# Performance work log

Measured on AMD Instinct MI355X. Metric: run time of the kernel, lower is better.

Reference implementation:

```python
import jax, jax.numpy as jnp
import numpy as np

B, S, V, M = 8, 512, 32000, 32
PAD_ID = 1


def setup_inputs() -> dict:
    key = jax.random.key(0)
    k1, k2, k3 = jax.random.split(key, 3)
    logits = jax.random.normal(k1, (B, S, V), dtype=jnp.float32)
    a = jax.random.randint(k2, (B, S), 0, V, dtype=jnp.int64)
    mask = jax.random.randint(k3, (B, S, M), 0, V, dtype=jnp.int64)
    return {"logits": logits, "a": a, "mask": mask}


def reference(logits, a, mask):
    # softmax over vocab: prob[b,s,v]
    prob = jax.nn.softmax(logits, axis=-1)
    # _base: masked gather + segment-sum over candidate ids (>0 are valid)
    gathered = jnp.take_along_axis(prob, mask, axis=-1)      # [B,S,M]
    valid = (mask > 0).astype(prob.dtype)
    base = (gathered * valid).sum(-1)                         # [B,S]
    # prob of the taken action token (equiv. to one_hot * prob sum)
    p_a = jnp.take_along_axis(prob, a[..., None], axis=-1)[..., 0]  # [B,S]
    logp = jnp.log(p_a / base)
    pad_mask = (a != PAD_ID).astype(prob.dtype)
    return (logp * pad_mask).sum(-1)                          # [B]
```

## Files before the change

kernel.cpp:

```cpp
#include <hip/hip_runtime.h>
#include <hip/hip_bf16.h>
#include <math.h>


#define BB 8
#define SS 512
#define VV 32000
#define MM 32

__global__ void init_out_kernel(float* out) {
    if (threadIdx.x < BB) out[threadIdx.x] = 0.0f;
}

__global__ __launch_bounds__(256) void logp_kernel(
    const float* __restrict__ logits,
    const int*   __restrict__ a,
    const int*   __restrict__ mask,
    float*       __restrict__ out)
{
    const int wave = threadIdx.x >> 6;
    const int lane = threadIdx.x & 63;
    const int pos  = (blockIdx.x << 2) + wave;
    const int b    = pos >> 9;

    const float* __restrict__ row = logits + (size_t)pos * VV;

    const int aid = a[pos];
    const float logit_a = row[aid];

    float x = -INFINITY;
    if (lane < MM) {
        const int m = mask[pos * MM + lane];
        if (m > 0) x = row[m];
    }

    float mx = x;
    #pragma unroll
    for (int off = 32; off; off >>= 1)
        mx = fmaxf(mx, __shfl_xor(mx, off, 64));

    float e = (x == -INFINITY) ? 0.0f : expf(x - mx);
    #pragma unroll
    for (int off = 32; off; off >>= 1)
        e += __shfl_xor(e, off, 64);

    const float lse  = mx + logf(e);
    const float logp = (aid != 1) ? (logit_a - lse) : 0.0f;

    __shared__ float ws[4];
    if (lane == 0) ws[wave] = logp;
    __syncthreads();
    if (threadIdx.x == 0) {
        const float s = ws[0] + ws[1] + ws[2] + ws[3];
        atomicAdd(&out[b], s);
    }
}

extern "C" void kernel_launch(void* const* d_in, const int* in_sizes, int n_in,
                              void* d_out, int out_size, void* d_ws, size_t ws_size,
                              hipStream_t stream) {
    const float* logits = (const float*)d_in[0];
    const int*   a      = (const int*)d_in[1];
    const int*   mask   = (const int*)d_in[2];
    float*       out    = (float*)d_out;

    init_out_kernel<<<1, 64, 0, stream>>>(out);

    const int n_pos  = BB * SS;
    const int blocks = n_pos / 4;
    logp_kernel<<<blocks, 256, 0, stream>>>(logits, a, mask, out);
}
```

Before: 564.5 us.

## Fuse output init into one block-per-batch kernel with per-position loop

```diff
diff --git a/kernel.cpp b/kernel.cpp
--- a/kernel.cpp
+++ b/kernel.cpp
@@ -8,51 +8,63 @@
 #define VV 32000
 #define MM 32
 
-__global__ void init_out_kernel(float* out) {
-    if (threadIdx.x < BB) out[threadIdx.x] = 0.0f;
-}
-
-__global__ __launch_bounds__(256) void logp_kernel(
+__global__ __launch_bounds__(1024) void logp_fused_kernel(
     const float* __restrict__ logits,
     const int*   __restrict__ a,
     const int*   __restrict__ mask,
     float*       __restrict__ out)
 {
+    const int b    = blockIdx.x;
     const int wave = threadIdx.x >> 6;
     const int lane = threadIdx.x & 63;
-    const int pos  = (blockIdx.x << 2) + wave;
-    const int b    = pos >> 9;
+    const int hl   = lane & 31;
+    const int half = lane >> 5;
 
-    const float* __restrict__ row = logits + (size_t)pos * VV;
+    const int pos_base = b * SS + wave * 32 + half;
 
-    const int aid = a[pos];
-    const float logit_a = row[aid];
+    float acc = 0.0f;
 
-    float x = -INFINITY;
-    if (lane < MM) {
-        const int m = mask[pos * MM + lane];
-        if (m > 0) x = row[m];
+    int m_cur = mask[pos_base * MM + hl];
+    int a_cur = a[pos_base];
+
+    #pragma unroll
+    for (int i = 0; i < 16; ++i) {
+        const int pos = pos_base + 2 * i;
+        const float* __restrict__ row = logits + (size_t)pos * VV;
+
+        float x  = (m_cur > 0) ? row[m_cur] : -INFINITY;
+        float la = row[a_cur];
+        const int a_hold = a_cur;
+
+        if (i < 15) {
+            m_cur = mask[(pos + 2) * MM + hl];
+            a_cur = a[pos + 2];
+        }
+
+        float mx = x;
+        #pragma unroll
+        for (int off = 16; off; off >>= 1)
+            mx = fmaxf(mx, __shfl_xor(mx, off, 64));
+
+        float e = (x == -INFINITY) ? 0.0f : expf(x - mx);
+        #pragma unroll
+        for (int off = 16; off; off >>= 1)
+            e += __shfl_xor(e, off, 64);
+
+        const float lse = mx + logf(e);
+        if (hl == 0 && a_hold != 1) acc += la - lse;
     }
 
-    float mx = x;
-    #pragma unroll
-    for (int off = 32; off; off >>= 1)
-        mx = fmaxf(mx, __shfl_xor(mx, off, 64));
+    acc += __shfl_xor(acc, 32, 64);
 
-    float e = (x == -INFINITY) ? 0.0f : expf(x - mx);
-    #pragma unroll
-    for (int off = 32; off; off >>= 1)
-        e += __shfl_xor(e, off, 64);
-
-    const float lse  = mx + logf(e);
-    const float logp = (aid != 1) ? (logit_a - lse) : 0.0f;
-
-    __shared__ float ws[4];
-    if (lane == 0) ws[wave] = logp;
+    __shared__ float wsum[16];
+    if (lane == 0) wsum[wave] = acc;
     __syncthreads();
     if (threadIdx.x == 0) {
-        const float s = ws[0] + ws[1] + ws[2] + ws[3];
-        atomicAdd(&out[b], s);
+        float s = 0.0f;
+        #pragma unroll
+        for (int w = 0; w < 16; ++w) s += wsum[w];
+        out[b] = s;
     }
 }
 
@@ -64,9 +76,5 @@
     const int*   mask   = (const int*)d_in[2];
     float*       out    = (float*)d_out;
 
-    init_out_kernel<<<1, 64, 0, stream>>>(out);
-
-    const int n_pos  = BB * SS;
-    const int blocks = n_pos / 4;
-    logp_kernel<<<blocks, 256, 0, stream>>>(logits, a, mask, out);
+    logp_fused_kernel<<<BB, 1024, 0, stream>>>(logits, a, mask, out);
 }
```

After: 594.3 us. 1.05x slower.

## Assign one block per batch row and one thread per position, dropping atomics

Applied to the files above, without the earlier changes.

```diff
diff --git a/kernel.cpp b/kernel.cpp
--- a/kernel.cpp
+++ b/kernel.cpp
@@ -8,51 +8,62 @@
 #define VV 32000
 #define MM 32
 
-__global__ void init_out_kernel(float* out) {
-    if (threadIdx.x < BB) out[threadIdx.x] = 0.0f;
-}
-
-__global__ __launch_bounds__(256) void logp_kernel(
+__global__ __launch_bounds__(512) void logp_kernel(
     const float* __restrict__ logits,
     const int*   __restrict__ a,
     const int*   __restrict__ mask,
     float*       __restrict__ out)
 {
-    const int wave = threadIdx.x >> 6;
-    const int lane = threadIdx.x & 63;
-    const int pos  = (blockIdx.x << 2) + wave;
-    const int b    = pos >> 9;
+    const int b   = blockIdx.x;
+    const int t   = threadIdx.x;
+    const int pos = b * SS + t;
 
     const float* __restrict__ row = logits + (size_t)pos * VV;
 
-    const int aid = a[pos];
-    const float logit_a = row[aid];
-
-    float x = -INFINITY;
-    if (lane < MM) {
-        const int m = mask[pos * MM + lane];
-        if (m > 0) x = row[m];
+    const int a_id = a[pos];
+    int m[MM];
+    const int4* __restrict__ mrow = reinterpret_cast<const int4*>(mask + (size_t)pos * MM);
+    #pragma unroll
+    for (int q = 0; q < MM / 4; ++q) {
+        const int4 v = mrow[q];
+        m[4 * q + 0] = v.x; m[4 * q + 1] = v.y;
+        m[4 * q + 2] = v.z; m[4 * q + 3] = v.w;
     }
 
-    float mx = x;
+    float x[MM];
+    #pragma unroll
+    for (int j = 0; j < MM; ++j) {
+        const int idx = (m[j] > 0) ? m[j] : 0;
+        x[j] = row[idx];
+    }
+    const float logit_a = row[a_id];
+
+    float mx = -INFINITY;
+    #pragma unroll
+    for (int j = 0; j < MM; ++j)
+        mx = fmaxf(mx, (m[j] > 0) ? x[j] : -INFINITY);
+
+    float e = 0.0f;
+    #pragma unroll
+    for (int j = 0; j < MM; ++j)
+        e += (m[j] > 0) ? expf(x[j] - mx) : 0.0f;
+
+    const float lse  = mx + logf(e);
+    float logp = (a_id != 1) ? (logit_a - lse) : 0.0f;
+
     #pragma unroll
     for (int off = 32; off; off >>= 1)
-        mx = fmaxf(mx, __shfl_xor(mx, off, 64));
+        logp += __shfl_xor(logp, off, 64);
 
-    float e = (x == -INFINITY) ? 0.0f : expf(x - mx);
-    #pragma unroll
-    for (int off = 32; off; off >>= 1)
-        e += __shfl_xor(e, off, 64);
-
-    const float lse  = mx + logf(e);
-    const float logp = (aid != 1) ? (logit_a - lse) : 0.0f;
-
-    __shared__ float ws[4];
-    if (lane == 0) ws[wave] = logp;
+    __shared__ float wsum[8];
+    const int wave = t >> 6;
+    if ((t & 63) == 0) wsum[wave] = logp;
     __syncthreads();
-    if (threadIdx.x == 0) {
-        const float s = ws[0] + ws[1] + ws[2] + ws[3];
-        atomicAdd(&out[b], s);
+    if (t == 0) {
+        float s = 0.0f;
+        #pragma unroll
+        for (int w = 0; w < 8; ++w) s += wsum[w];
+        out[b] = s;
     }
 }
 
@@ -64,9 +75,5 @@
     const int*   mask   = (const int*)d_in[2];
     float*       out    = (float*)d_out;
 
-    init_out_kernel<<<1, 64, 0, stream>>>(out);
-
-    const int n_pos  = BB * SS;
-    const int blocks = n_pos / 4;
-    logp_kernel<<<blocks, 256, 0, stream>>>(logits, a, mask, out);
+    logp_kernel<<<BB, SS, 0, stream>>>(logits, a, mask, out);
 }
```

After: 598.9 us. +6.1%, slower.
